# Kernel optimization log

Hardware: AMD Instinct MI355X
Metric: run time of the kernel (lower is better)

## Reference

```python
import jax, jax.numpy as jnp
import numpy as np

N, L, D = 256, 512, 512


def _attention(x, W_in, W_out, apply_tanh):
    # x: [N, L, D]; 'general' attention: project query, score against context (=x)
    q = jnp.einsum('bld,ed->ble', x, W_in)          # [N, L, D]
    scores = jnp.einsum('bld,bmd->blm', q, x)       # [N, L, L]
    w = jax.nn.softmax(scores, axis=-1)             # softmax over keys
    mix = jnp.einsum('blm,bmd->bld', w, x)          # [N, L, D]
    comb = jnp.concatenate([mix, q], axis=-1)       # [N, L, 2D]
    out = jnp.einsum('blc,dc->bld', comb, W_out)    # Linear(2D, D), no bias
    return jnp.tanh(out) if apply_tanh else out


def setup_inputs() -> dict:
    key = jax.random.key(0)
    k1, k2, k3, k4, k5 = jax.random.split(key, 5)
    s = 0.02
    return {
        'embeddings': jax.random.normal(k1, (N, L, D), dtype=jnp.float32),
        'W_in1': jax.random.normal(k2, (D, D), dtype=jnp.float32) * s,
        'W_out1': jax.random.normal(k3, (D, 2 * D), dtype=jnp.float32) * s,
        'W_in2': jax.random.normal(k4, (D, D), dtype=jnp.float32) * s,
        'W_out2': jax.random.normal(k5, (D, 2 * D), dtype=jnp.float32) * s,
    }


def reference(embeddings, W_in1, W_out1, W_in2, W_out2):
    x = _attention(embeddings, W_in1, W_out1, apply_tanh=True)   # block 1 (tanh)
    x = _attention(x, W_in2, W_out2, apply_tanh=False)           # block 2 (no tanh)
    # transpose(1,2) + avg_pool1d over full length == mean over L
    pooled = jnp.mean(x, axis=1)                                  # [N, D]
    return pooled.reshape(pooled.shape[0], -1, 1, 1)              # [N, D, 1, 1]
```

## Files before the change

### kernel.cpp

```cpp
#include <hip/hip_runtime.h>
#include <cstdint>
#include <cstddef>

typedef uint16_t u16;
typedef __attribute__((ext_vector_type(8))) short bf16x8;
typedef __attribute__((ext_vector_type(4))) float f32x4;
typedef __attribute__((ext_vector_type(4))) uint16_t u16x4;

#define GLOBAL_AS(p) (const __attribute__((address_space(1))) void*)(p)
#define LDS_AS(p)    (__attribute__((address_space(3))) void*)(p)

__device__ __forceinline__ void bar_vm4(){
  asm volatile("s_waitcnt vmcnt(4)" ::: "memory");
  __builtin_amdgcn_s_barrier();
  asm volatile("" ::: "memory");
}
__device__ __forceinline__ void bar_vm0(){
  asm volatile("s_waitcnt vmcnt(0)" ::: "memory");
  __builtin_amdgcn_s_barrier();
  asm volatile("" ::: "memory");
}
__device__ __forceinline__ void bar_end(){
  asm volatile("" ::: "memory");
  __builtin_amdgcn_s_barrier();
  asm volatile("" ::: "memory");
}
__device__ __forceinline__ void bar_lgkm(){
  asm volatile("s_waitcnt lgkmcnt(0)" ::: "memory");
  __builtin_amdgcn_s_barrier();
  asm volatile("" ::: "memory");
}

__device__ __forceinline__ u16 f2b(float f){
  uint32_t u = __float_as_uint(f);
  u += 0x7fff + ((u >> 16) & 1);
  return (u16)(u >> 16);
}

__global__ void cvt_bf16_kernel(const float* __restrict__ src, u16* __restrict__ dst, int n){
  int i = (blockIdx.x * 256 + threadIdx.x) * 4;
  if (i >= n) return;
  float4 f = *(const float4*)(src + i);
  u16x4 o; o.x = f2b(f.x); o.y = f2b(f.y); o.z = f2b(f.z); o.w = f2b(f.w);
  *(u16x4*)(dst + i) = o;
}

__global__ void cvtT_kernel(const float* __restrict__ src, u16* __restrict__ x, u16* __restrict__ xT){
  __shared__ u16 tile[64][68];
  size_t b = blockIdx.y;
  int t = blockIdx.x;
  int r0 = (t >> 3) * 64, c0 = (t & 7) * 64;
  const float* s = src + b * 262144;
  u16* dx = x + b * 262144;
  u16* dT = xT + b * 262144;
  int tx = threadIdx.x & 63, ty = threadIdx.x >> 6;
  #pragma unroll
  for (int k = 0; k < 16; k++){
    int r = ty * 16 + k;
    u16 v = f2b(s[(size_t)(r0 + r) * 512 + c0 + tx]);
    dx[(size_t)(r0 + r) * 512 + c0 + tx] = v;
    tile[r][tx] = v;
  }
  __syncthreads();
  #pragma unroll
  for (int k = 0; k < 16; k++){
    int c = ty * 16 + k;
    dT[(size_t)(c0 + c) * 512 + r0 + tx] = tile[tx][c];
  }
}

__global__ void transpose512_kernel(const u16* __restrict__ src, u16* __restrict__ dst){
  __shared__ u16 tile[64][68];
  size_t b = blockIdx.y;
  int t = blockIdx.x;
  int r0 = (t >> 3) * 64, c0 = (t & 7) * 64;
  const u16* s = src + b * 262144;
  u16* d = dst + b * 262144;
  int tx = threadIdx.x & 63, ty = threadIdx.x >> 6;
  #pragma unroll
  for (int k = 0; k < 16; k++){
    int r = ty * 16 + k;
    tile[r][tx] = s[(size_t)(r0 + r) * 512 + c0 + tx];
  }
  __syncthreads();
  #pragma unroll
  for (int k = 0; k < 16; k++){
    int c = ty * 16 + k;
    d[(size_t)(c0 + c) * 512 + r0 + tx] = tile[tx][c];
  }
}

__global__ __launch_bounds__(512, 2) void attn_kernel(
    const u16* __restrict__ q, const u16* __restrict__ x, const u16* __restrict__ xT,
    u16* __restrict__ mix, int batPerXcd)
{
  __shared__ __align__(16) u16 U[64 * 520];
  __shared__ __align__(16) u16 Bx[2][512 * 32];
  __shared__ float stats[2][64][8];
  const int64_t E = 262144;
  int id = blockIdx.x;
  int tile = (id >> 3) & 7;
  int64_t bat = (int64_t)(id & 7) * batPerXcd + (id >> 6);
  q += bat * E; x += bat * E; xT += bat * E; mix += bat * E;
  int m0 = tile * 64;
  int tid = threadIdx.x, lane = tid & 63, w = tid >> 6;
  int fr = lane & 15, qd = lane >> 4;
  int fq = qd * 8;
  int sw = ((tid & 3) ^ ((tid >> 3) & 3)) * 8;
  int bslot = (qd ^ ((fr >> 1) & 3)) * 8;

  auto stage = [&](const u16* __restrict__ src, int buf, int k0){
    #pragma unroll
    for (int s = 0; s < 4; s++){
      const u16* g = src + (size_t)(s * 128 + (tid >> 2)) * 512 + k0 + sw;
      __builtin_amdgcn_global_load_lds(GLOBAL_AS(g), LDS_AS(&Bx[buf][s * 4096 + tid * 8]), 16, 0, 0);
    }
  };

  stage(x, 0, 0);

  #pragma unroll
  for (int c = 0; c < 8; c++){
    int row = c * 8 + w;
    __builtin_amdgcn_global_load_lds(GLOBAL_AS(q + (size_t)(m0 + row) * 512 + lane * 8),
                                     LDS_AS(&U[row * 520 + lane * 8]), 16, 0, 0);
  }

  f32x4 acc[4][4];
  #pragma unroll
  for (int i = 0; i < 4; i++)
    #pragma unroll
    for (int j = 0; j < 4; j++) acc[i][j] = (f32x4){0.f, 0.f, 0.f, 0.f};

  for (int it = 0; it < 16; ++it){
    if (it < 15) stage(x, (it + 1) & 1, (it + 1) * 32);
    else         stage(xT, 0, 0);
    bar_vm4();
    int k0 = it * 32;
    bf16x8 af[4], bfr[4];
    #pragma unroll
    for (int i = 0; i < 4; i++) af[i]  = *(const bf16x8*)&U[(i * 16 + fr) * 520 + k0 + fq];
    #pragma unroll
    for (int j = 0; j < 4; j++) bfr[j] = *(const bf16x8*)&Bx[it & 1][(w * 64 + j * 16 + fr) * 32 + bslot];
    #pragma unroll
    for (int i = 0; i < 4; i++)
      #pragma unroll
      for (int j = 0; j < 4; j++)
        acc[i][j] = __builtin_amdgcn_mfma_f32_16x16x32_bf16(af[i], bfr[j], acc[i][j], 0, 0, 0);
    bar_end();
  }

  float inv[4][4];
  #pragma unroll
  for (int i = 0; i < 4; i++)
    #pragma unroll
    for (int r = 0; r < 4; r++){
      float m = acc[i][0][r];
      #pragma unroll
      for (int j = 1; j < 4; j++) m = fmaxf(m, acc[i][j][r]);
      #pragma unroll
      for (int o = 1; o <= 8; o <<= 1) m = fmaxf(m, __shfl_xor(m, o));
      if (fr == 0) stats[0][i * 16 + qd * 4 + r][w] = m;
    }
  bar_lgkm();
  #pragma unroll
  for (int i = 0; i < 4; i++)
    #pragma unroll
    for (int r = 0; r < 4; r++){
      int row = i * 16 + qd * 4 + r;
      float m = stats[0][row][0];
      #pragma unroll
      for (int t = 1; t < 8; t++) m = fmaxf(m, stats[0][row][t]);
      float s = 0.f;
      #pragma unroll
      for (int j = 0; j < 4; j++){
        float e = __expf(acc[i][j][r] - m);
        acc[i][j][r] = e; s += e;
      }
      #pragma unroll
      for (int o = 1; o <= 8; o <<= 1) s += __shfl_xor(s, o);
      if (fr == 0) stats[1][row][w] = s;
    }
  bar_lgkm();
  #pragma unroll
  for (int i = 0; i < 4; i++)
    #pragma unroll
    for (int r = 0; r < 4; r++){
      int row = i * 16 + qd * 4 + r;
      float s = stats[1][row][0];
      #pragma unroll
      for (int t = 1; t < 8; t++) s += stats[1][row][t];
      inv[i][r] = 1.0f / s;
    }
  #pragma unroll
  for (int i = 0; i < 4; i++)
    #pragma unroll
    for (int r = 0; r < 4; r++)
      #pragma unroll
      for (int j = 0; j < 4; j++){
        int row = i * 16 + qd * 4 + r;
        int col = w * 64 + j * 16 + fr;
        uint32_t mine = f2b(acc[i][j][r] * inv[i][r]);
        uint32_t oth = (uint32_t)__shfl_xor((int)mine, 1);
        if (!(fr & 1)) *(uint32_t*)&U[row * 520 + col] = mine | (oth << 16);
      }
  bar_lgkm();

  #pragma unroll
  for (int i = 0; i < 4; i++)
    #pragma unroll
    for (int j = 0; j < 4; j++) acc[i][j] = (f32x4){0.f, 0.f, 0.f, 0.f};
  for (int it = 0; it < 16; ++it){
    if (it < 15){ stage(xT, (it + 1) & 1, (it + 1) * 32); bar_vm4(); }
    else        { bar_vm0(); }
    int k0 = it * 32;
    bf16x8 af[4], bfr[4];
    #pragma unroll
    for (int i = 0; i < 4; i++) af[i]  = *(const bf16x8*)&U[(i * 16 + fr) * 520 + k0 + fq];
    #pragma unroll
    for (int j = 0; j < 4; j++) bfr[j] = *(const bf16x8*)&Bx[it & 1][(w * 64 + j * 16 + fr) * 32 + bslot];
    #pragma unroll
    for (int i = 0; i < 4; i++)
      #pragma unroll
      for (int j = 0; j < 4; j++)
        acc[i][j] = __builtin_amdgcn_mfma_f32_16x16x32_bf16(af[i], bfr[j], acc[i][j], 0, 0, 0);
    bar_end();
  }
  #pragma unroll
  for (int i = 0; i < 4; i++)
    #pragma unroll
    for (int j = 0; j < 4; j++)
      #pragma unroll
      for (int r = 0; r < 4; r++)
        mix[(size_t)(m0 + i * 16 + qd * 4 + r) * 512 + w * 64 + j * 16 + fr] =
            f2b(acc[i][j][r]);
}

template<bool SPLIT, bool TANH, bool POOL, typename CT>
__global__ __launch_bounds__(256, 2) void gemm_bt_kernel(
    const u16* __restrict__ A0, const u16* __restrict__ A1,
    const u16* __restrict__ B, CT* __restrict__ C,
    int K, int ldb, int64_t aBatch, int64_t bBatch, int64_t cBatch,
    float* __restrict__ poolOut, int b0)
{
  __shared__ __align__(16) u16 As[2][128 * 32];
  __shared__ __align__(16) u16 Bs[2][128 * 32];
  int64_t bat = blockIdx.y;
  int m0 = (blockIdx.x & 3) * 128, n0 = (blockIdx.x >> 2) * 128;
  A0 += bat * aBatch;
  if (SPLIT) A1 += bat * aBatch;
  B += bat * bBatch;
  if (!POOL) C += bat * cBatch;
  int tid = threadIdx.x, lane = tid & 63;
  int w = tid >> 6;
  int wm = (w >> 1) * 64, wn = (w & 1) * 64;
  f32x4 acc[4][4];
  #pragma unroll
  for (int i = 0; i < 4; i++)
    #pragma unroll
    for (int j = 0; j < 4; j++) acc[i][j] = (f32x4){0.f, 0.f, 0.f, 0.f};

  int sRow = tid >> 2;
  int sCol = ((tid & 3) ^ ((tid >> 3) & 3)) * 8;
  int fr = lane & 15;
  int fq = ((lane >> 4) ^ ((fr >> 1) & 3)) * 8;

  auto stageG = [&](int buf, int k0){
    const u16* Ap = A0; int kk = k0;
    if (SPLIT && k0 >= 512){ Ap = A1; kk = k0 - 512; }
    const u16* ga = Ap + (size_t)(m0 + sRow) * 512 + kk + sCol;
    const u16* gb = B  + (size_t)(n0 + sRow) * ldb + k0 + sCol;
    __builtin_amdgcn_global_load_lds(GLOBAL_AS(ga),                    LDS_AS(&As[buf][tid * 8]),        16, 0, 0);
    __builtin_amdgcn_global_load_lds(GLOBAL_AS(ga + (size_t)64 * 512), LDS_AS(&As[buf][2048 + tid * 8]), 16, 0, 0);
    __builtin_amdgcn_global_load_lds(GLOBAL_AS(gb),                    LDS_AS(&Bs[buf][tid * 8]),        16, 0, 0);
    __builtin_amdgcn_global_load_lds(GLOBAL_AS(gb + (size_t)64 * ldb), LDS_AS(&Bs[buf][2048 + tid * 8]), 16, 0, 0);
  };

  stageG(0, 0);

  int nIt = K >> 5;
  for (int it = 0; it < nIt; ++it){
    if (it + 1 < nIt){ stageG((it + 1) & 1, (it + 1) * 32); bar_vm4(); }
    else             { bar_vm0(); }
    bf16x8 af[4], bfr[4];
    #pragma unroll
    for (int i = 0; i < 4; i++) af[i]  = *(const bf16x8*)&As[it & 1][(wm + i * 16 + fr) * 32 + fq];
    #pragma unroll
    for (int j = 0; j < 4; j++) bfr[j] = *(const bf16x8*)&Bs[it & 1][(wn + j * 16 + fr) * 32 + fq];
    #pragma unroll
    for (int i = 0; i < 4; i++)
      #pragma unroll
      for (int j = 0; j < 4; j++)
        acc[i][j] = __builtin_amdgcn_mfma_f32_16x16x32_bf16(af[i], bfr[j], acc[i][j], 0, 0, 0);
    bar_end();
  }

  if constexpr (POOL){
    #pragma unroll
    for (int j = 0; j < 4; j++){
      float p = 0.f;
      #pragma unroll
      for (int i = 0; i < 4; i++)
        #pragma unroll
        for (int r = 0; r < 4; r++) p += acc[i][j][r];
      p += __shfl_xor(p, 16);
      p += __shfl_xor(p, 32);
      if (lane < 16){
        int col = n0 + wn + j * 16 + lane;
        atomicAdd(poolOut + ((size_t)(b0) + bat) * 512 + col, p * (1.0f / 512.0f));
      }
    }
  } else {
    int cq = (lane >> 4) * 4, cc = lane & 15;
    #pragma unroll
    for (int i = 0; i < 4; i++){
      #pragma unroll
      for (int j = 0; j < 4; j++){
        #pragma unroll
        for (int r = 0; r < 4; r++){
          int row = m0 + wm + i * 16 + cq + r;
          int col = n0 + wn + j * 16 + cc;
          float v = acc[i][j][r];
          if (TANH) v = tanhf(v);
          if constexpr (sizeof(CT) == 4) C[(size_t)row * 512 + col] = v;
          else                           C[(size_t)row * 512 + col] = f2b(v);
        }
      }
    }
  }
}

extern "C" void kernel_launch(void* const* d_in, const int* in_sizes, int n_in,
                              void* d_out, int out_size, void* d_ws, size_t ws_size,
                              hipStream_t stream) {
  const float* emb   = (const float*)d_in[0];
  const float* Win1  = (const float*)d_in[1];
  const float* Wout1 = (const float*)d_in[2];
  const float* Win2  = (const float*)d_in[3];
  const float* Wout2 = (const float*)d_in[4];
  float* out = (float*)d_out;

  int CB = 256;
  while (CB > 8 && (4ull << 20) + (size_t)CB * (5ull * 524288ull) > ws_size) CB >>= 1;
  const int64_t E = 262144;

  char* wsb = (char*)d_ws;
  u16* Win1b  = (u16*)wsb;
  u16* Wout1b = Win1b + 262144;
  u16* Win2b  = Wout1b + 524288;
  u16* Wout2b = Win2b + 262144;
  u16* base = (u16*)(wsb + (4 << 20));
  u16* Ar = base;
  u16* Br = base + (size_t)CB * E;
  u16* Cr = base + 2 * (size_t)CB * E;
  u16* Dr = base + 3 * (size_t)CB * E;
  u16* Fr = base + 4 * (size_t)CB * E;

  hipMemsetAsync(d_out, 0, (size_t)out_size * sizeof(float), stream);

  cvt_bf16_kernel<<<256, 256, 0, stream>>>(Win1,  Win1b,  262144);
  cvt_bf16_kernel<<<512, 256, 0, stream>>>(Wout1, Wout1b, 524288);
  cvt_bf16_kernel<<<256, 256, 0, stream>>>(Win2,  Win2b,  262144);
  cvt_bf16_kernel<<<512, 256, 0, stream>>>(Wout2, Wout2b, 524288);

  dim3 gg(16, CB);
  dim3 gt(64, CB);
  int nAttnBlocks = CB * 8;
  int batPerXcd = CB / 8;

  for (int c = 0; c < 256 / CB; c++){
    const float* embc = emb + (size_t)c * CB * 262144;
    int b0 = c * CB;

    cvtT_kernel<<<gt, 256, 0, stream>>>(embc, Ar, Cr);
    gemm_bt_kernel<false,false,false,u16><<<gg, 256, 0, stream>>>(
        Ar, nullptr, Win1b, Br, 512, 512, E, 0, E, nullptr, 0);
    attn_kernel<<<nAttnBlocks, 512, 0, stream>>>(Br, Ar, Cr, Fr, batPerXcd);
    gemm_bt_kernel<true,true,false,u16><<<gg, 256, 0, stream>>>(
        Fr, Br, Wout1b, Dr, 1024, 1024, E, 0, E, nullptr, 0);

    transpose512_kernel<<<gt, 256, 0, stream>>>(Dr, Cr);
    gemm_bt_kernel<false,false,false,u16><<<gg, 256, 0, stream>>>(
        Dr, nullptr, Win2b, Ar, 512, 512, E, 0, E, nullptr, 0);
    attn_kernel<<<nAttnBlocks, 512, 0, stream>>>(Ar, Dr, Cr, Fr, batPerXcd);
    gemm_bt_kernel<true,false,true,u16><<<gg, 256, 0, stream>>>(
        Fr, Ar, Wout2b, (u16*)nullptr, 1024, 1024, E, 0, 0, out, b0);
  }
}
```

Measured before the change: 1.709 ms.

## Make attention B-tile staging wave-private and drop per-iteration block barriers

Restructures the x/xT staging in the attention kernel so each wave loads only the 64 rows it consumes into its own LDS slice, with swizzle applied per wave. That lets the two K-loops drop the block-wide barriers in favour of per-wave vmcnt/lgkmcnt waits. The prefetch becomes distance-2: buffers are preloaded, then each buffer is refilled right after its fragments are read, and both loops are fully unrolled. This removes s_barrier stalls and lets waves drift apart, at the cost of relying on careful per-wave waitcnt ordering for correctness.

```diff
diff --git a/kernel.cpp b/kernel.cpp
--- a/kernel.cpp
+++ b/kernel.cpp
@@ -95,7 +95,7 @@
     u16* __restrict__ mix, int batPerXcd)
 {
   __shared__ __align__(16) u16 U[64 * 520];
-  __shared__ __align__(16) u16 Bx[2][512 * 32];
+  __shared__ __align__(16) u16 Bx[2][8][64 * 32];
   __shared__ float stats[2][64][8];
   const int64_t E = 262144;
   int id = blockIdx.x;
@@ -106,18 +106,17 @@
   int tid = threadIdx.x, lane = tid & 63, w = tid >> 6;
   int fr = lane & 15, qd = lane >> 4;
   int fq = qd * 8;
-  int sw = ((tid & 3) ^ ((tid >> 3) & 3)) * 8;
   int bslot = (qd ^ ((fr >> 1) & 3)) * 8;
 
   auto stage = [&](const u16* __restrict__ src, int buf, int k0){
     #pragma unroll
     for (int s = 0; s < 4; s++){
-      const u16* g = src + (size_t)(s * 128 + (tid >> 2)) * 512 + k0 + sw;
-      __builtin_amdgcn_global_load_lds(GLOBAL_AS(g), LDS_AS(&Bx[buf][s * 4096 + tid * 8]), 16, 0, 0);
+      int rloc = s * 16 + (lane >> 2);
+      int chunk = (lane & 3) ^ ((rloc >> 1) & 3);
+      const u16* g = src + (size_t)(w * 64 + rloc) * 512 + k0 + chunk * 8;
+      __builtin_amdgcn_global_load_lds(GLOBAL_AS(g), LDS_AS(&Bx[buf][w][s * 512 + lane * 8]), 16, 0, 0);
     }
   };
-
-  stage(x, 0, 0);
 
   #pragma unroll
   for (int c = 0; c < 8; c++){
@@ -125,6 +124,11 @@
     __builtin_amdgcn_global_load_lds(GLOBAL_AS(q + (size_t)(m0 + row) * 512 + lane * 8),
                                      LDS_AS(&U[row * 520 + lane * 8]), 16, 0, 0);
   }
+  stage(x, 0, 0);
+  stage(x, 1, 32);
+  asm volatile("s_waitcnt vmcnt(8)" ::: "memory");
+  __builtin_amdgcn_s_barrier();
+  asm volatile("" ::: "memory");
 
   f32x4 acc[4][4];
   #pragma unroll
@@ -132,22 +136,24 @@
     #pragma unroll
     for (int j = 0; j < 4; j++) acc[i][j] = (f32x4){0.f, 0.f, 0.f, 0.f};
 
+  #pragma unroll
   for (int it = 0; it < 16; ++it){
-    if (it < 15) stage(x, (it + 1) & 1, (it + 1) * 32);
-    else         stage(xT, 0, 0);
-    bar_vm4();
+    asm volatile("s_waitcnt vmcnt(4)" ::: "memory");
     int k0 = it * 32;
     bf16x8 af[4], bfr[4];
     #pragma unroll
     for (int i = 0; i < 4; i++) af[i]  = *(const bf16x8*)&U[(i * 16 + fr) * 520 + k0 + fq];
     #pragma unroll
-    for (int j = 0; j < 4; j++) bfr[j] = *(const bf16x8*)&Bx[it & 1][(w * 64 + j * 16 + fr) * 32 + bslot];
+    for (int j = 0; j < 4; j++) bfr[j] = *(const bf16x8*)&Bx[it & 1][w][(j * 16 + fr) * 32 + bslot];
+    asm volatile("s_waitcnt lgkmcnt(0)" ::: "memory");
+    if (it <= 13)      stage(x,  it & 1, (it + 2) * 32);
+    else if (it == 14) stage(xT, 0, 0);
+    else               stage(xT, 1, 32);
     #pragma unroll
     for (int i = 0; i < 4; i++)
       #pragma unroll
       for (int j = 0; j < 4; j++)
         acc[i][j] = __builtin_amdgcn_mfma_f32_16x16x32_bf16(af[i], bfr[j], acc[i][j], 0, 0, 0);
-    bar_end();
   }
 
   float inv[4][4];
@@ -210,21 +216,23 @@
   for (int i = 0; i < 4; i++)
     #pragma unroll
     for (int j = 0; j < 4; j++) acc[i][j] = (f32x4){0.f, 0.f, 0.f, 0.f};
+  #pragma unroll
   for (int it = 0; it < 16; ++it){
-    if (it < 15){ stage(xT, (it + 1) & 1, (it + 1) * 32); bar_vm4(); }
-    else        { bar_vm0(); }
+    if (it < 15) asm volatile("s_waitcnt vmcnt(4)" ::: "memory");
+    else         asm volatile("s_waitcnt vmcnt(0)" ::: "memory");
     int k0 = it * 32;
     bf16x8 af[4], bfr[4];
     #pragma unroll
     for (int i = 0; i < 4; i++) af[i]  = *(const bf16x8*)&U[(i * 16 + fr) * 520 + k0 + fq];
     #pragma unroll
-    for (int j = 0; j < 4; j++) bfr[j] = *(const bf16x8*)&Bx[it & 1][(w * 64 + j * 16 + fr) * 32 + bslot];
+    for (int j = 0; j < 4; j++) bfr[j] = *(const bf16x8*)&Bx[it & 1][w][(j * 16 + fr) * 32 + bslot];
+    asm volatile("s_waitcnt lgkmcnt(0)" ::: "memory");
+    if (it <= 13) stage(xT, it & 1, (it + 2) * 32);
     #pragma unroll
     for (int i = 0; i < 4; i++)
       #pragma unroll
       for (int j = 0; j < 4; j++)
         acc[i][j] = __builtin_amdgcn_mfma_f32_16x16x32_bf16(af[i], bfr[j], acc[i][j], 0, 0, 0);
-    bar_end();
   }
   #pragma unroll
   for (int i = 0; i < 4; i++)
```

After: 1.632 ms. 4.5% less time.
